# Kernel tuning notes

Measured on AMD Instinct MI355X. Metric: run time of the kernel, lower is better.

The kernel has to match this reference:

```python
import jax, jax.numpy as jnp
import numpy as np

D_IN = 1024
D_OUT = 1024
N_HEADS = 16
D_K = D_OUT // N_HEADS
ROPE_THETA = 10000.0


def setup_inputs() -> dict:
    key = jax.random.key(0)
    ks = jax.random.split(key, 5)
    x = jax.random.normal(ks[0], (2, 2048, D_IN), dtype=jnp.float32)
    token_positions = jnp.arange(2048, dtype=jnp.int32)
    scale = 0.02
    wq = jax.random.normal(ks[1], (D_OUT, D_IN), dtype=jnp.float32) * scale
    wk = jax.random.normal(ks[2], (D_OUT, D_IN), dtype=jnp.float32) * scale
    wv = jax.random.normal(ks[3], (D_OUT, D_IN), dtype=jnp.float32) * scale
    wo = jax.random.normal(ks[4], (D_OUT, D_OUT), dtype=jnp.float32) * scale
    return {"x": x, "token_positions": token_positions, "wq": wq, "wk": wk, "wv": wv, "wo": wo}


def _rope(x, token_positions):
    # x: [..., S, d_k]; token_positions: [S]
    d_k = x.shape[-1]
    idx = jnp.arange(d_k)
    k = idx // 2
    # thetas[i, j] = pos_i / theta^(2*(j//2)/d_k)
    angles = token_positions[:, None].astype(x.dtype) / jnp.power(
        jnp.asarray(ROPE_THETA, x.dtype), 2.0 * k.astype(x.dtype) / d_k
    )  # [S, d_k]
    cos = jnp.cos(angles)
    sin = jnp.sin(angles) * jnp.where(idx % 2 == 0, -1.0, 1.0).astype(x.dtype)
    pair_swaps = idx + jnp.where(idx % 2 == 0, 1, -1)  # swap even/odd pairs
    return x * cos + x[..., pair_swaps] * sin


def _forward(x, token_positions, wq, wk, wv, wo):
    B, S, _ = x.shape
    # fused QKV projection (same math as concat + split)
    q = jnp.einsum("bsd,od->bso", x, wq)
    k = jnp.einsum("bsd,od->bso", x, wk)
    v = jnp.einsum("bsd,od->bso", x, wv)
    # split heads: [B, S, H*dk] -> [B, H, S, dk]
    split = lambda t: t.reshape(B, S, N_HEADS, D_K).transpose(0, 2, 1, 3)
    q, k, v = split(q), split(k), split(v)
    q = _rope(q, token_positions)
    k = _rope(k, token_positions)
    scores = jnp.einsum("bhqd,bhkd->bhqk", q, k) / jnp.sqrt(jnp.asarray(D_K, x.dtype))
    causal = jnp.tril(jnp.ones((S, S), dtype=bool))
    scores = jnp.where(causal, scores, -jnp.inf)
    probs = jax.nn.softmax(scores, axis=-1)
    ctx = jnp.einsum("bhqk,bhkd->bhqd", probs, v)
    merged = ctx.transpose(0, 2, 1, 3).reshape(B, S, D_OUT)
    return jnp.einsum("bsm,om->bso", merged, wo)


def reference(x, token_positions, wq, wk, wv, wo):
    return _forward(x, token_positions, wq, wk, wv, wo)
```

## Files before the change

kernel.cpp:

```cpp
#include <hip/hip_runtime.h>

#define D_MODEL 1024
#define SEQ     2048
#define BATCH   2
#define NHEADS  16
#define DK      64
#define NROWS   (BATCH*SEQ)

typedef unsigned short u16;
typedef __bf16 bf16x8 __attribute__((ext_vector_type(8)));
typedef float  f32x4  __attribute__((ext_vector_type(4)));

__device__ __forceinline__ u16 f2bf(float f) {
    union { float f; unsigned u; } v; v.f = f;
    unsigned u = v.u;
    u += 0x7fffu + ((u >> 16) & 1);
    return (u16)(u >> 16);
}
__device__ __forceinline__ float bf2f(u16 h) {
    union { unsigned u; float f; } v; v.u = ((unsigned)h) << 16;
    return v.f;
}

__device__ __forceinline__ void gload_lds16(const u16* g, u16* l) {
    __builtin_amdgcn_global_load_lds(
        (const __attribute__((address_space(1))) void*)g,
        (__attribute__((address_space(3))) void*)l, 16, 0, 0);
}

__global__ void cvt_bf16_all(const float* __restrict__ x,
                             const float* __restrict__ w0, const float* __restrict__ w1,
                             const float* __restrict__ w2, const float* __restrict__ w3,
                             u16* __restrict__ xb, u16* __restrict__ wb) {
    int i = blockIdx.x * blockDim.x + threadIdx.x;
    int row = i >> 8;
    int c   = (i & 255) * 4;
    const float* src; u16* dst;
    if (row < 4096) {
        src = x + (size_t)row * 1024;
        dst = xb + (size_t)row * 1024;
    } else {
        int r2 = row - 4096;
        int ws = r2 >> 10;
        int rr = r2 & 1023;
        const float* wsrc = ws == 0 ? w0 : ws == 1 ? w1 : ws == 2 ? w2 : w3;
        src = wsrc + (size_t)rr * 1024;
        dst = wb + ((size_t)ws << 20) + (size_t)rr * 1024;
    }
    float4 v = *(const float4*)(src + c);
    uint2 o;
    o.x = (unsigned)f2bf(v.x) | ((unsigned)f2bf(v.y) << 16);
    o.y = (unsigned)f2bf(v.z) | ((unsigned)f2bf(v.w) << 16);
    *(uint2*)(dst + c) = o;
}

__global__ __launch_bounds__(256) void gemm_qkv_p(
    const u16* __restrict__ A, const u16* __restrict__ W,
    u16* __restrict__ Qp, u16* __restrict__ Kp, u16* __restrict__ Vt)
{
    __shared__ __align__(16) u16 Ash[128 * 32];
    __shared__ __align__(16) u16 Bsh[128 * 32];

    const int m0  = blockIdx.x * 128;
    const int sel = blockIdx.y >> 3;
    const int n0  = (blockIdx.y & 7) * 128;
    const u16* B = W + ((size_t)sel << 20);
    const int tid = threadIdx.x;
    const int lane = tid & 63;
    const int w    = tid >> 6;
    const int wr = w >> 1, wc = w & 1;
    const int fr = lane & 15;
    const int fk = (lane >> 4) * 8;
    const int rsub = lane >> 2;
    const int csub = (lane & 3) * 8;

    f32x4 acc[4][4];
#pragma unroll
    for (int i = 0; i < 4; ++i)
#pragma unroll
        for (int j = 0; j < 4; ++j) acc[i][j] = (f32x4){0.f, 0.f, 0.f, 0.f};

    for (int k0 = 0; k0 < 1024; k0 += 32) {
        __syncthreads();
        const u16* Ab = A + (size_t)(m0 + 16 * w + rsub) * 1024 + k0 + csub;
        const u16* Bb = B + (size_t)(n0 + 16 * w + rsub) * 1024 + k0 + csub;
#pragma unroll
        for (int half = 0; half < 2; ++half) {
            size_t ro = (size_t)(half * 64) * 1024;
            int lo = (half * 64 + 16 * w) * 32;
            gload_lds16(Ab + ro, &Ash[lo]);
            gload_lds16(Bb + ro, &Bsh[lo]);
        }
        __syncthreads();

        bf16x8 ah[4], bh[4];
#pragma unroll
        for (int i = 0; i < 4; ++i)
            ah[i] = *(const bf16x8*)&Ash[(wr * 64 + i * 16 + fr) * 32 + fk];
#pragma unroll
        for (int j = 0; j < 4; ++j)
            bh[j] = *(const bf16x8*)&Bsh[(wc * 64 + j * 16 + fr) * 32 + fk];
#pragma unroll
        for (int i = 0; i < 4; ++i)
#pragma unroll
            for (int j = 0; j < 4; ++j)
                acc[i][j] = __builtin_amdgcn_mfma_f32_16x16x32_bf16(ah[i], bh[j], acc[i][j], 0, 0, 0);
    }

    const int r0 = (lane >> 4) * 4;
#pragma unroll
    for (int i = 0; i < 4; ++i) {
#pragma unroll
        for (int j = 0; j < 4; ++j) {
            int col = n0 + wc * 64 + j * 16 + fr;
#pragma unroll
            for (int r = 0; r < 4; ++r) {
                int row = m0 + wr * 64 + i * 16 + r0 + r;
                u16 v = f2bf(acc[i][j][r]);
                if (sel == 0)      Qp[(size_t)row * 1024 + col] = v;
                else if (sel == 1) Kp[(size_t)row * 1024 + col] = v;
                else               Vt[(size_t)col * NROWS + row] = v;
            }
        }
    }
}

__global__ __launch_bounds__(256) void gemm_out_p(
    const u16* __restrict__ A, const u16* __restrict__ B, float* __restrict__ Cout)
{
    __shared__ __align__(16) u16 Ash[128 * 32];
    __shared__ __align__(16) u16 Bsh[128 * 32];

    const int m0 = blockIdx.x * 128;
    const int n0 = blockIdx.y * 128;
    const int tid = threadIdx.x;
    const int lane = tid & 63;
    const int w    = tid >> 6;
    const int wr = w >> 1, wc = w & 1;
    const int fr = lane & 15;
    const int fk = (lane >> 4) * 8;
    const int rsub = lane >> 2;
    const int csub = (lane & 3) * 8;

    f32x4 acc[4][4];
#pragma unroll
    for (int i = 0; i < 4; ++i)
#pragma unroll
        for (int j = 0; j < 4; ++j) acc[i][j] = (f32x4){0.f, 0.f, 0.f, 0.f};

    for (int k0 = 0; k0 < 1024; k0 += 32) {
        __syncthreads();
        const u16* Ab = A + (size_t)(m0 + 16 * w + rsub) * 1024 + k0 + csub;
        const u16* Bb = B + (size_t)(n0 + 16 * w + rsub) * 1024 + k0 + csub;
#pragma unroll
        for (int half = 0; half < 2; ++half) {
            size_t ro = (size_t)(half * 64) * 1024;
            int lo = (half * 64 + 16 * w) * 32;
            gload_lds16(Ab + ro, &Ash[lo]);
            gload_lds16(Bb + ro, &Bsh[lo]);
        }
        __syncthreads();

        bf16x8 ah[4], bh[4];
#pragma unroll
        for (int i = 0; i < 4; ++i)
            ah[i] = *(const bf16x8*)&Ash[(wr * 64 + i * 16 + fr) * 32 + fk];
#pragma unroll
        for (int j = 0; j < 4; ++j)
            bh[j] = *(const bf16x8*)&Bsh[(wc * 64 + j * 16 + fr) * 32 + fk];
#pragma unroll
        for (int i = 0; i < 4; ++i)
#pragma unroll
            for (int j = 0; j < 4; ++j)
                acc[i][j] = __builtin_amdgcn_mfma_f32_16x16x32_bf16(ah[i], bh[j], acc[i][j], 0, 0, 0);
    }

    const int r0 = (lane >> 4) * 4;
#pragma unroll
    for (int i = 0; i < 4; ++i) {
#pragma unroll
        for (int j = 0; j < 4; ++j) {
            int col = n0 + wc * 64 + j * 16 + fr;
#pragma unroll
            for (int r = 0; r < 4; ++r)
                Cout[(size_t)(m0 + wr * 64 + i * 16 + r0 + r) * 1024 + col] = acc[i][j][r];
        }
    }
}

__global__ void rope_plain(u16* __restrict__ qk, const int* __restrict__ pos) {
    int i = blockIdx.x * blockDim.x + threadIdx.x;
    int p = i & 511;
    int n = i >> 9;
    int s = n & 2047;
    int k = p & 31;
    int h = p >> 5;
    size_t base = (size_t)n * 1024 + h * DK + 2 * k;
    unsigned v = *(const unsigned*)&qk[base];
    float x0 = bf2f((u16)(v & 0xffff));
    float x1 = bf2f((u16)(v >> 16));
    float ang = (float)pos[s] * expf((float)k * -0.28782313662425575f);
    float c = cosf(ang), sn = sinf(ang);
    float y0 = x0 * c - x1 * sn;
    float y1 = x1 * c + x0 * sn;
    *(unsigned*)&qk[base] = (unsigned)f2bf(y0) | ((unsigned)f2bf(y1) << 16);
}

__global__ __launch_bounds__(512, 4) void attn_v6(
    const u16* __restrict__ Qp, const u16* __restrict__ Kp, const u16* __restrict__ Vt,
    u16* __restrict__ Op, float* __restrict__ mlbuf)
{
    const int slot = 39 - (int)blockIdx.x;
    const int h = blockIdx.y, b = blockIdx.z;
    int g, rr;
    if (slot < 4)       { g = 0; rr = slot; }
    else if (slot < 12) { g = 1; rr = slot - 4; }
    else if (slot < 24) { g = 2; rr = slot - 12; }
    else                { g = 3; rr = slot - 24; }
    const int qq  = rr / (g + 1);
    const int qt2 = 4 * g + qq;
    const int c   = rr - qq * (g + 1);

    const int tid  = threadIdx.x;
    const int lane = tid & 63;
    const int w    = tid >> 6;
    const int fr = lane & 15;
    const int fg = lane >> 4;
    const int bS = b * SEQ;
    const int hd = h * DK;
    const int qbase = qt2 * 128 + 16 * w;
    const int ntk = 2 * qt2 + 2;
    const int kt0 = 8 * c;
    const int kt1 = min(8 * c + 8, ntk);

    __shared__ __align__(16) u16 Kl[2][64 * 64];
    __shared__ __align__(16) u16 Vl[2][64 * 64];
    __shared__ __align__(16) u16 Plds[8][16][72];

    const int srow = 8 * w + (lane >> 3);
    const int scol = (((lane & 7) ^ (lane >> 3)) * 8);
    const int swz  = (fr & 7) * 8;

    const u16* qrow = Qp + (size_t)(bS + qbase + fr) * 1024 + hd;
    bf16x8 qf0 = *(const bf16x8*)(qrow + fg * 8);
    bf16x8 qf1 = *(const bf16x8*)(qrow + 32 + fg * 8);

    f32x4 o[4];
#pragma unroll
    for (int j = 0; j < 4; ++j) o[j] = (f32x4){0.f, 0.f, 0.f, 0.f};
    float mrow = -1e30f, lrow = 0.f;

#define STAGE(BUF, KT) do { \
    int kb_ = (KT) * 64; \
    gload_lds16(Kp + (size_t)(bS + kb_ + srow) * 1024 + hd + scol, &Kl[BUF][(8 * w) * 64]); \
    gload_lds16(Vt + (size_t)(hd + srow) * NROWS + bS + kb_ + scol, &Vl[BUF][(8 * w) * 64]); \
} while (0)

    STAGE(0, kt0);
    __syncthreads();

    int cur = 0;
    for (int kt = kt0; kt < kt1; ++kt) {
        if (kt + 1 < kt1) STAGE(cur ^ 1, kt + 1);
        const int k0 = kt * 64;
        if (k0 <= qbase + 15) {
            bf16x8 kf[4][2];
#pragma unroll
            for (int t = 0; t < 4; ++t) {
                const u16* kr = &Kl[cur][(16 * t + fr) * 64];
                kf[t][0] = *(const bf16x8*)(kr + ((fg * 8) ^ swz));
                kf[t][1] = *(const bf16x8*)(kr + (((4 + fg) * 8) ^ swz));
            }
            f32x4 sc4[4];
#pragma unroll
            for (int t = 0; t < 4; ++t) {
                f32x4 a = (f32x4){0.f, 0.f, 0.f, 0.f};
                a = __builtin_amdgcn_mfma_f32_16x16x32_bf16(kf[t][0], qf0, a, 0, 0, 0);
                a = __builtin_amdgcn_mfma_f32_16x16x32_bf16(kf[t][1], qf1, a, 0, 0, 0);
                sc4[t] = a;
            }
            float p[4][4];
            if (k0 + 63 > qbase) {
#pragma unroll
                for (int t = 0; t < 4; ++t)
#pragma unroll
                    for (int r = 0; r < 4; ++r) {
                        float v = sc4[t][r] * 0.125f;
                        if (k0 + 16 * t + 4 * fg + r > qbase + fr) v = -1e30f;
                        p[t][r] = v;
                    }
            } else {
#pragma unroll
                for (int t = 0; t < 4; ++t)
#pragma unroll
                    for (int r = 0; r < 4; ++r) p[t][r] = sc4[t][r] * 0.125f;
            }
            float mx = p[0][0];
#pragma unroll
            for (int t = 0; t < 4; ++t)
#pragma unroll
                for (int r = 0; r < 4; ++r) mx = fmaxf(mx, p[t][r]);
            mx = fmaxf(mx, __shfl_xor(mx, 16));
            mx = fmaxf(mx, __shfl_xor(mx, 32));
            float mnew = fmaxf(mrow, mx);
            float scf = __expf(mrow - mnew);
            mrow = mnew;
            float rs = 0.f;
#pragma unroll
            for (int t = 0; t < 4; ++t)
#pragma unroll
                for (int r = 0; r < 4; ++r) {
                    p[t][r] = __expf(p[t][r] - mnew);
                    rs += p[t][r];
                }
            rs += __shfl_xor(rs, 16);
            rs += __shfl_xor(rs, 32);
            lrow = lrow * scf + rs;
            float scr[4];
#pragma unroll
            for (int r = 0; r < 4; ++r) scr[r] = __shfl(scf, 4 * fg + r);
#pragma unroll
            for (int j = 0; j < 4; ++j)
#pragma unroll
                for (int r = 0; r < 4; ++r) o[j][r] *= scr[r];
#pragma unroll
            for (int t = 0; t < 4; ++t)
#pragma unroll
                for (int r = 0; r < 4; ++r)
                    Plds[w][fr][16 * t + 4 * fg + r] = f2bf(p[t][r]);
            bf16x8 pf0 = *(const bf16x8*)&Plds[w][fr][fg * 8];
            bf16x8 pf1 = *(const bf16x8*)&Plds[w][fr][32 + fg * 8];
#pragma unroll
            for (int j = 0; j < 4; ++j) {
                const u16* vr = &Vl[cur][(16 * j + fr) * 64];
                bf16x8 v0 = *(const bf16x8*)(vr + ((fg * 8) ^ swz));
                bf16x8 v1 = *(const bf16x8*)(vr + (((4 + fg) * 8) ^ swz));
                o[j] = __builtin_amdgcn_mfma_f32_16x16x32_bf16(pf0, v0, o[j], 0, 0, 0);
                o[j] = __builtin_amdgcn_mfma_f32_16x16x32_bf16(pf1, v1, o[j], 0, 0, 0);
            }
        }
        __syncthreads();
        cur ^= 1;
    }
#undef STAGE

    const int slotg = (b * NHEADS + h) * 40 + slot;
#pragma unroll
    for (int r = 0; r < 4; ++r) {
        int rrel = 16 * w + 4 * fg + r;
#pragma unroll
        for (int j = 0; j < 4; ++j)
            Op[((size_t)slotg * 128 + rrel) * 64 + 16 * j + fr] = f2bf(o[j][r]);
    }
    if (fg == 0) {
        float* pp = mlbuf + ((size_t)slotg * 128 + 16 * w + fr) * 2;
        pp[0] = mrow;
        pp[1] = lrow;
    }
}

__global__ void attn_combine3(const u16* __restrict__ Op, const float* __restrict__ mlbuf,
                              u16* __restrict__ Mb) {
    int i = blockIdx.x * blockDim.x + threadIdx.x;
    int row = i >> 7;
    int c8  = (i & 127) * 8;
    int h   = c8 >> 6;
    int s   = row & 2047;
    int b   = row >> 11;
    int qt2 = s >> 7;
    int g   = qt2 >> 2;
    int nch = g + 1;
    int slot0 = (b * NHEADS + h) * 40 + 2 * g * (g + 1) + (qt2 & 3) * (g + 1);
    int rrel = s & 127, crel = c8 & 63;

    float mv[4], lv[4];
    float m = -1e30f;
    for (int k = 0; k < nch; ++k) {
        const float* pp = mlbuf + ((size_t)(slot0 + k) * 128 + rrel) * 2;
        mv[k] = pp[0]; lv[k] = pp[1];
        m = fmaxf(m, mv[k]);
    }
    float L = 0.f;
    for (int k = 0; k < nch; ++k) {
        mv[k] = __expf(mv[k] - m);
        L += lv[k] * mv[k];
    }
    float acc[8];
#pragma unroll
    for (int jj = 0; jj < 8; ++jj) acc[jj] = 0.f;
    for (int k = 0; k < nch; ++k) {
        float wgt = mv[k];
        uint4 u = *(const uint4*)(Op + ((size_t)(slot0 + k) * 128 + rrel) * 64 + crel);
        const unsigned* wrd = (const unsigned*)&u;
#pragma unroll
        for (int kk = 0; kk < 4; ++kk) {
            acc[2 * kk]     += wgt * bf2f((u16)(wrd[kk] & 0xffff));
            acc[2 * kk + 1] += wgt * bf2f((u16)(wrd[kk] >> 16));
        }
    }
    float inv = 1.0f / L;
    unsigned ou[4];
#pragma unroll
    for (int kk = 0; kk < 4; ++kk)
        ou[kk] = (unsigned)f2bf(acc[2 * kk] * inv) | ((unsigned)f2bf(acc[2 * kk + 1] * inv) << 16);
    *(uint4*)(Mb + (size_t)row * 1024 + c8) = *(uint4*)ou;
}

extern "C" void kernel_launch(void* const* d_in, const int* in_sizes, int n_in,
                              void* d_out, int out_size, void* d_ws, size_t ws_size,
                              hipStream_t stream) {
    const float* x   = (const float*)d_in[0];
    const int*   pos = (const int*)d_in[1];
    const float* wq  = (const float*)d_in[2];
    const float* wk  = (const float*)d_in[3];
    const float* wv  = (const float*)d_in[4];
    const float* wo  = (const float*)d_in[5];
    float* out = (float*)d_out;

    char* ws = (char*)d_ws;
    u16* xb  = (u16*)(ws);
    u16* wb  = (u16*)(ws + (24ull << 20));
    u16* wob = wb + 3 * (1 << 20);
    u16* Qp  = (u16*)(ws + (32ull << 20));
    u16* Kp  = (u16*)(ws + (40ull << 20));
    u16* Vt  = (u16*)(ws + (48ull << 20));
    u16* Mb  = (u16*)(ws + (56ull << 20));
    u16* Op  = (u16*)(ws);
    float* mlbuf = (float*)(ws + (21ull << 20));

    cvt_bf16_all<<<8192, 256, 0, stream>>>(x, wq, wk, wv, wo, xb, wb);

    gemm_qkv_p<<<dim3(NROWS / 128, 24), 256, 0, stream>>>(xb, wb, Qp, Kp, Vt);

    rope_plain<<<16384, 256, 0, stream>>>(Qp, pos);

    attn_v6<<<dim3(40, NHEADS, BATCH), 512, 0, stream>>>(Qp, Kp, Vt, Op, mlbuf);
    attn_combine3<<<2048, 256, 0, stream>>>(Op, mlbuf, Mb);

    gemm_out_p<<<dim3(NROWS / 128, 8), 256, 0, stream>>>(Mb, wob, out);
}
```

Baseline: 153.5 us.

## Fold softmax scale and log2e into Q, use exp2 with lazy rescale

Q is prescaled during RoPE by 1/sqrt(dk)*log2(e), which removes the per-score multiply and lets the softmax use exp2f. The output accumulator is rescaled only when some row maximum grows by more than 8 (in log2 units), so most tiles skip the rescale shuffles and multiplies. P is packed to bf16 with v_cvt_pk_bf16_f32 and written with vector stores, and the max reduction becomes a tree. The trade-off is looser numerics: stale maxima let exp2 values reach up to 2^8, and Q is now stored pre-scaled in bf16.

New measurement: 155.5 us. About the same (+1.3%).

```diff
diff --git a/kernel.cpp b/kernel.cpp
--- a/kernel.cpp
+++ b/kernel.cpp
@@ -20,6 +20,11 @@
 __device__ __forceinline__ float bf2f(u16 h) {
     union { unsigned u; float f; } v; v.u = ((unsigned)h) << 16;
     return v.f;
+}
+__device__ __forceinline__ unsigned cvtpk_bf16(float lo, float hi) {
+    unsigned r;
+    asm("v_cvt_pk_bf16_f32 %0, %1, %2" : "=v"(r) : "v"(lo), "v"(hi));
+    return r;
 }
 
 __device__ __forceinline__ void gload_lds16(const u16* g, u16* l) {
@@ -201,12 +206,14 @@
     float x1 = bf2f((u16)(v >> 16));
     float ang = (float)pos[s] * expf((float)k * -0.28782313662425575f);
     float c = cosf(ang), sn = sinf(ang);
+    float qs = (n < 4096) ? 0.18033688011112042f : 1.0f;
+    c *= qs; sn *= qs;
     float y0 = x0 * c - x1 * sn;
     float y1 = x1 * c + x0 * sn;
     *(unsigned*)&qk[base] = (unsigned)f2bf(y0) | ((unsigned)f2bf(y1) << 16);
 }
 
-__global__ __launch_bounds__(512, 4) void attn_v6(
+__global__ __launch_bounds__(512, 4) void attn_v7(
     const u16* __restrict__ Qp, const u16* __restrict__ Kp, const u16* __restrict__ Vt,
     u16* __restrict__ Op, float* __restrict__ mlbuf)
 {
@@ -280,54 +287,56 @@
                 sc4[t] = a;
             }
             float p[4][4];
+#pragma unroll
+            for (int t = 0; t < 4; ++t)
+#pragma unroll
+                for (int r = 0; r < 4; ++r) p[t][r] = sc4[t][r];
             if (k0 + 63 > qbase) {
 #pragma unroll
                 for (int t = 0; t < 4; ++t)
 #pragma unroll
-                    for (int r = 0; r < 4; ++r) {
-                        float v = sc4[t][r] * 0.125f;
-                        if (k0 + 16 * t + 4 * fg + r > qbase + fr) v = -1e30f;
-                        p[t][r] = v;
-                    }
-            } else {
-#pragma unroll
-                for (int t = 0; t < 4; ++t)
-#pragma unroll
-                    for (int r = 0; r < 4; ++r) p[t][r] = sc4[t][r] * 0.125f;
-            }
-            float mx = p[0][0];
-#pragma unroll
-            for (int t = 0; t < 4; ++t)
-#pragma unroll
-                for (int r = 0; r < 4; ++r) mx = fmaxf(mx, p[t][r]);
+                    for (int r = 0; r < 4; ++r)
+                        if (k0 + 16 * t + 4 * fg + r > qbase + fr) p[t][r] = -1e30f;
+            }
+            float a0 = fmaxf(fmaxf(p[0][0], p[0][1]), fmaxf(p[0][2], p[0][3]));
+            float a1 = fmaxf(fmaxf(p[1][0], p[1][1]), fmaxf(p[1][2], p[1][3]));
+            float a2 = fmaxf(fmaxf(p[2][0], p[2][1]), fmaxf(p[2][2], p[2][3]));
+            float a3 = fmaxf(fmaxf(p[3][0], p[3][1]), fmaxf(p[3][2], p[3][3]));
+            float mx = fmaxf(fmaxf(a0, a1), fmaxf(a2, a3));
             mx = fmaxf(mx, __shfl_xor(mx, 16));
             mx = fmaxf(mx, __shfl_xor(mx, 32));
-            float mnew = fmaxf(mrow, mx);
-            float scf = __expf(mrow - mnew);
-            mrow = mnew;
+            float scf = 1.0f;
+            if (!__all(mx <= mrow + 8.0f)) {
+                float mnew = fmaxf(mrow, mx);
+                scf = exp2f(mrow - mnew);
+                float s0 = __shfl(scf, 4 * fg);
+                float s1 = __shfl(scf, 4 * fg + 1);
+                float s2 = __shfl(scf, 4 * fg + 2);
+                float s3 = __shfl(scf, 4 * fg + 3);
+#pragma unroll
+                for (int j = 0; j < 4; ++j) {
+                    o[j][0] *= s0; o[j][1] *= s1; o[j][2] *= s2; o[j][3] *= s3;
+                }
+                mrow = mnew;
+            }
             float rs = 0.f;
 #pragma unroll
             for (int t = 0; t < 4; ++t)
 #pragma unroll
                 for (int r = 0; r < 4; ++r) {
-                    p[t][r] = __expf(p[t][r] - mnew);
+                    p[t][r] = exp2f(p[t][r] - mrow);
                     rs += p[t][r];
                 }
             rs += __shfl_xor(rs, 16);
             rs += __shfl_xor(rs, 32);
             lrow = lrow * scf + rs;
-            float scr[4];
-#pragma unroll
-            for (int r = 0; r < 4; ++r) scr[r] = __shfl(scf, 4 * fg + r);
-#pragma unroll
-            for (int j = 0; j < 4; ++j)
-#pragma unroll
-                for (int r = 0; r < 4; ++r) o[j][r] *= scr[r];
-#pragma unroll
-            for (int t = 0; t < 4; ++t)
-#pragma unroll
-                for (int r = 0; r < 4; ++r)
-                    Plds[w][fr][16 * t + 4 * fg + r] = f2bf(p[t][r]);
+#pragma unroll
+            for (int t = 0; t < 4; ++t) {
+                uint2 pk;
+                pk.x = cvtpk_bf16(p[t][0], p[t][1]);
+                pk.y = cvtpk_bf16(p[t][2], p[t][3]);
+                *(uint2*)&Plds[w][fr][16 * t + 4 * fg] = pk;
+            }
             bf16x8 pf0 = *(const bf16x8*)&Plds[w][fr][fg * 8];
             bf16x8 pf1 = *(const bf16x8*)&Plds[w][fr][32 + fg * 8];
 #pragma unroll
@@ -382,7 +391,7 @@
     }
     float L = 0.f;
     for (int k = 0; k < nch; ++k) {
-        mv[k] = __expf(mv[k] - m);
+        mv[k] = exp2f(mv[k] - m);
         L += lv[k] * mv[k];
     }
     float acc[8];
@@ -434,7 +443,7 @@
 
     rope_plain<<<16384, 256, 0, stream>>>(Qp, pos);
 
-    attn_v6<<<dim3(40, NHEADS, BATCH), 512, 0, stream>>>(Qp, Kp, Vt, Op, mlbuf);
+    attn_v7<<<dim3(40, NHEADS, BATCH), 512, 0, stream>>>(Qp, Kp, Vt, Op, mlbuf);
     attn_combine3<<<2048, 256, 0, stream>>>(Op, mlbuf, Mb);
 
     gemm_out_p<<<dim3(NROWS / 128, 8), 256, 0, stream>>>(Mb, wob, out);
```
